# Performance work log

Hardware: AMD Instinct MI355X
Metric: run time of the kernel (lower is better)

## Reference

```python
import jax, jax.numpy as jnp
import numpy as np

N_NODES = 50000
N_EDGES = 800000
IN_DIM = 128
HID = 32
HEADS = 4


def _lin_init(key, fan_in, fan_out):
    k1, k2 = jax.random.split(key)
    s = 1.0 / np.sqrt(fan_in)
    W = jax.random.uniform(k1, (fan_in, fan_out), jnp.float32, -s, s)
    b = jax.random.uniform(k2, (fan_out,), jnp.float32, -s, s)
    return W, b


def setup_inputs() -> dict:
    key = jax.random.key(0)
    keys = jax.random.split(key, 12)
    x = jax.random.normal(keys[0], (N_NODES, IN_DIM), jnp.float32)
    edge_index = jax.random.randint(keys[1], (2, N_EDGES), 0, N_NODES, jnp.int64)

    # conv1: in_dim -> heads*hid (128 -> 4*32)
    Wq1, bq1 = _lin_init(keys[2], IN_DIM, HEADS * HID)
    Wk1, bk1 = _lin_init(keys[3], IN_DIM, HEADS * HID)
    Wv1, bv1 = _lin_init(keys[4], IN_DIM, HEADS * HID)
    Ws1, bs1 = _lin_init(keys[5], IN_DIM, HEADS * HID)
    # conv2: 128 -> 1*32
    Wq2, bq2 = _lin_init(keys[6], HEADS * HID, HID)
    Wk2, bk2 = _lin_init(keys[7], HEADS * HID, HID)
    Wv2, bv2 = _lin_init(keys[8], HEADS * HID, HID)
    Ws2, bs2 = _lin_init(keys[9], HEADS * HID, HID)
    # output linear: 32 -> 1
    Wo, bo = _lin_init(keys[10], HID, 1)

    return {
        "x": x, "edge_index": edge_index,
        "Wq1": Wq1, "bq1": bq1, "Wk1": Wk1, "bk1": bk1,
        "Wv1": Wv1, "bv1": bv1, "Ws1": Ws1, "bs1": bs1,
        "Wq2": Wq2, "bq2": bq2, "Wk2": Wk2, "bk2": bk2,
        "Wv2": Wv2, "bv2": bv2, "Ws2": Ws2, "bs2": bs2,
        "Wo": Wo, "bo": bo,
    }


def transformer_conv(x, edge_index, Wq, bq, Wk, bk, Wv, bv, Ws, bs, heads, d):
    # PyG TransformerConv (concat=True, root_weight=True, beta=False, no edge attr).
    n = x.shape[0]
    src, dst = edge_index[0], edge_index[1]  # message j(src) -> i(dst)
    q = (x @ Wq + bq).reshape(n, heads, d)
    k = (x @ Wk + bk).reshape(n, heads, d)
    v = (x @ Wv + bv).reshape(n, heads, d)
    # per-edge attention logits [E, heads]
    logits = (q[dst] * k[src]).sum(-1) / jnp.sqrt(jnp.float32(d))
    # segment softmax over incoming edges of each target node
    m = jax.ops.segment_max(logits, dst, num_segments=n)
    p = jnp.exp(logits - m[dst])
    denom = jax.ops.segment_sum(p, dst, num_segments=n)
    alpha = p / denom[dst]  # [E, heads]
    # weighted scatter-add of values
    msg = alpha[:, :, None] * v[src]  # [E, heads, d]
    aggr = jax.ops.segment_sum(msg, dst, num_segments=n).reshape(n, heads * d)
    return aggr + x @ Ws + bs  # root (skip) connection


def reference(x, edge_index,
              Wq1, bq1, Wk1, bk1, Wv1, bv1, Ws1, bs1,
              Wq2, bq2, Wk2, bk2, Wv2, bv2, Ws2, bs2,
              Wo, bo):
    h = transformer_conv(x, edge_index, Wq1, bq1, Wk1, bk1, Wv1, bv1, Ws1, bs1, HEADS, HID)
    h = jax.nn.relu(h)
    h = transformer_conv(h, edge_index, Wq2, bq2, Wk2, bk2, Wv2, bv2, Ws2, bs2, 1, HID)
    h = jax.nn.relu(h)
    g = h.mean(axis=0)  # [HID]
    return g @ Wo + bo  # [1]
```

## Files before the change

kernel.cpp:

```cpp
#include <hip/hip_runtime.h>
#include <math.h>

#define N_NODES 50000
#define N_EDGES 800000
#define NBK 196
#define BCAP 6144

typedef short short8 __attribute__((ext_vector_type(8)));
typedef float f32x4 __attribute__((ext_vector_type(4)));
typedef float f32x2 __attribute__((ext_vector_type(2)));

__device__ inline unsigned short f2bf(float v) {
  unsigned u = __float_as_uint(v);
  u += 0x7FFFu + ((u >> 16) & 1u);
  return (unsigned short)(u >> 16);
}
__device__ inline float bf2f(unsigned short b) {
  return __uint_as_float(((unsigned)b) << 16);
}
__device__ inline float bflo(unsigned u) { return __uint_as_float(u << 16); }
__device__ inline float bfhi(unsigned u) { return __uint_as_float(u & 0xFFFF0000u); }
__device__ inline unsigned char f2fp8(float v) {
  return (unsigned char)(__builtin_amdgcn_cvt_pk_fp8_f32(v, 0.f, 0, false) & 0xFF);
}
template <bool HI>
__device__ inline f32x2 fp8dec(unsigned u) {
  return __builtin_amdgcn_cvt_pk_f32_fp8(u, HI);
}

#define SCL 0.17677669529663687f

#define W1_B 256
#define W2_B 64
__global__ void prep_fused(const float* __restrict__ Wq1, const float* __restrict__ Wk1,
                           const float* __restrict__ Wv1, const float* __restrict__ Ws1,
                           const float* __restrict__ bq1, const float* __restrict__ bk1,
                           const float* __restrict__ bv1, const float* __restrict__ bs1,
                           const float* __restrict__ Wq2, const float* __restrict__ Wk2,
                           const float* __restrict__ Wv2, const float* __restrict__ Ws2,
                           const float* __restrict__ bq2, const float* __restrict__ bk2,
                           const float* __restrict__ bv2, const float* __restrict__ bs2,
                           unsigned short* __restrict__ Wt1, float* __restrict__ bcat1,
                           unsigned short* __restrict__ Wt2, float* __restrict__ bcat2,
                           const int* __restrict__ ei, int* __restrict__ bhist, int E) {
  const int b = blockIdx.x, tid = threadIdx.x;
  if (b < W1_B) {
    int i = b * 256 + tid;
    int c = i >> 7, k = i & 127;
    int mi = c >> 7, lc = c & 127;
    const float* W = (mi == 0) ? Wq1 : (mi == 1) ? Wk1 : (mi == 2) ? Wv1 : Ws1;
    float scl = (mi == 0) ? SCL : 1.f;
    Wt1[i] = f2bf(W[(size_t)k * 128 + lc] * scl);
    if (i < 512) {
      int bm = i >> 7, bl = i & 127;
      const float* bb = (bm == 0) ? bq1 : (bm == 1) ? bk1 : (bm == 2) ? bv1 : bs1;
      bcat1[i] = bb[bl] * ((bm == 0) ? SCL : 1.f);
    }
  } else if (b < W1_B + W2_B) {
    int i = (b - W1_B) * 256 + tid;
    int c = i >> 7, k = i & 127;
    int mi = c >> 5, lc = c & 31;
    const float* W = (mi == 0) ? Wq2 : (mi == 1) ? Wk2 : (mi == 2) ? Wv2 : Ws2;
    float scl = (mi == 0) ? SCL : 1.f;
    Wt2[i] = f2bf(W[(size_t)k * 32 + lc] * scl);
    if (i < 128) {
      int bm = i >> 5, bl = i & 31;
      const float* bb = (bm == 0) ? bq2 : (bm == 1) ? bk2 : (bm == 2) ? bv2 : bs2;
      bcat2[i] = bb[bl] * ((bm == 0) ? SCL : 1.f);
    }
  } else {
    __shared__ int h[NBK];
    for (int i = tid; i < NBK; i += 256) h[i] = 0;
    __syncthreads();
    int e = (b - W1_B - W2_B) * 4096 + tid;
#pragma unroll
    for (int p = 0; p < 16; ++p, e += 256)
      if (e < E) atomicAdd(&h[ei[E + e] >> 8], 1);
    __syncthreads();
    for (int i = tid; i < NBK; i += 256)
      if (h[i]) atomicAdd(&bhist[i], h[i]);
  }
}

__global__ void bucket_scan(const int* __restrict__ bhist, int* __restrict__ boff,
                            int* __restrict__ bcur) {
  __shared__ int s[256];
  int t = threadIdx.x;
  int v = (t < NBK) ? bhist[t] : 0;
  s[t] = v;
  __syncthreads();
#pragma unroll
  for (int off = 1; off < 256; off <<= 1) {
    int u = (t >= off) ? s[t - off] : 0;
    __syncthreads();
    s[t] += u;
    __syncthreads();
  }
  if (t < NBK) {
    int excl = s[t] - v;
    boff[t] = excl;
    bcur[t] = excl;
  }
  if (t == NBK - 1) boff[NBK] = s[t];
}

__global__ __launch_bounds__(256) void scatter_gemm1(
    const int* __restrict__ ei, int* __restrict__ bcur, int* __restrict__ ebuck, int E, int EB,
    const float* __restrict__ X, const unsigned short* __restrict__ Wt,
    const float* __restrict__ bcat, unsigned short* __restrict__ Q1b,
    unsigned short* __restrict__ SK1, unsigned char* __restrict__ KV8, int M) {
  __shared__ __align__(16) unsigned char L[3][64 * 272];
  const int tid = threadIdx.x;

  if ((int)blockIdx.x < EB) {
    int* lh = (int*)L[0];
    for (int i = tid; i < NBK; i += 256) lh[i] = 0;
    __syncthreads();
    const int e0 = blockIdx.x * 4096;
    int pks[16], bks[16];
#pragma unroll
    for (int p = 0; p < 16; ++p) {
      int e = e0 + p * 256 + tid;
      if (e < E) {
        int src = ei[e], dst = ei[E + e];
        pks[p] = (src << 8) | (dst & 255);
        bks[p] = dst >> 8;
        atomicAdd(&lh[bks[p]], 1);
      } else bks[p] = -1;
    }
    __syncthreads();
    for (int i = tid; i < NBK; i += 256)
      if (lh[i]) lh[i] = atomicAdd(&bcur[i], lh[i]);
    __syncthreads();
#pragma unroll
    for (int p = 0; p < 16; ++p) {
      if (bks[p] >= 0) {
        int slot = atomicAdd(&lh[bks[p]], 1);
        ebuck[slot] = pks[p];
      }
    }
    return;
  }

  unsigned short* As = (unsigned short*)L[0];
  const int bm = (blockIdx.x - EB) * 64;
  const int wave = tid >> 6, lane = tid & 63;
  const int lr = lane & 15, q = lane >> 4;

#pragma unroll
  for (int p = 0; p < 8; ++p) {
    int f = tid + p * 256;
    int row = f >> 5, c4 = f & 31;
    int gm = bm + row; if (gm >= M) gm = 0;
    float4 v = *(const float4*)(X + (size_t)gm * 128 + c4 * 4);
    ushort4 o;
    o.x = f2bf(v.x); o.y = f2bf(v.y); o.z = f2bf(v.z); o.w = f2bf(v.w);
    *(ushort4*)&As[row * 136 + c4 * 4] = o;
  }
  __syncthreads();

  const int colbase = wave * 128;
  f32x4 acc[4][8];
#pragma unroll
  for (int i = 0; i < 4; ++i)
#pragma unroll
    for (int j = 0; j < 8; ++j) acc[i][j] = (f32x4){0.f, 0.f, 0.f, 0.f};

#pragma unroll
  for (int ks = 0; ks < 4; ++ks) {
    short8 af[4];
#pragma unroll
    for (int i = 0; i < 4; ++i)
      af[i] = *(short8*)&As[(i * 16 + lr) * 136 + ks * 32 + q * 8];
#pragma unroll
    for (int j = 0; j < 8; ++j) {
      short8 bf = *(const short8*)(Wt + (size_t)(colbase + j * 16 + lr) * 128 + ks * 32 + q * 8);
#pragma unroll
      for (int i = 0; i < 4; ++i)
        acc[i][j] = __builtin_amdgcn_mfma_f32_16x16x32_bf16(af[i], bf, acc[i][j], 0, 0, 0);
    }
  }
  __syncthreads();

  float bj[8];
#pragma unroll
  for (int j = 0; j < 8; ++j) bj[j] = bcat[colbase + j * 16 + lr];

  if (wave == 0 || wave == 3) {
    unsigned short* Ls16 = (unsigned short*)((wave == 0) ? L[1] : L[0]);
#pragma unroll
    for (int i = 0; i < 4; ++i)
#pragma unroll
      for (int r = 0; r < 4; ++r) {
        int row = i * 16 + q * 4 + r;
#pragma unroll
        for (int j = 0; j < 8; ++j)
          Ls16[row * 136 + j * 16 + lr] = f2bf(acc[i][j][r] + bj[j]);
      }
  } else {
    unsigned char* KLs = L[2];
    const int voff = (wave == 2) ? 2 : 0;
#pragma unroll
    for (int i = 0; i < 4; ++i)
#pragma unroll
      for (int r = 0; r < 4; ++r) {
        int row = i * 16 + q * 4 + r;
#pragma unroll
        for (int j = 0; j < 8; ++j) {
          int d = j * 16 + lr;
          KLs[row * 272 + 4 * (d >> 1) + voff + (d & 1)] = f2fp8(acc[i][j][r] + bj[j]);
        }
      }
  }
  __syncthreads();

#pragma unroll
  for (int p = 0; p < 4; ++p) {
    int f = tid + p * 256;
    int row = f >> 4, u = f & 15;
    int gr = bm + row;
    if (gr < M) {
      *(uint4*)(Q1b + (size_t)gr * 128 + u * 8) = *(uint4*)&((unsigned short*)L[1])[row * 136 + u * 8];
      *(uint4*)(KV8 + (size_t)gr * 256 + u * 16) = *(uint4*)&L[2][row * 272 + u * 16];
      *(uint4*)(SK1 + (size_t)gr * 128 + u * 8) = *(uint4*)&((unsigned short*)L[0])[row * 136 + u * 8];
    }
  }
}

__global__ void bucket_csr(const int* __restrict__ ebuck, const int* __restrict__ boff,
                           int* __restrict__ rowptr, int* __restrict__ esrc, int N) {
  const int b = blockIdx.x;
  const int lo = boff[b], hi = boff[b + 1];
  const int cnt = hi - lo;
  __shared__ int hist[256];
  __shared__ int cur[256];
  __shared__ int sorted[BCAP];
  const int t = threadIdx.x;
  hist[t] = 0;
  __syncthreads();
  for (int i = t; i < cnt; i += 256) atomicAdd(&hist[ebuck[lo + i] & 255], 1);
  __syncthreads();
  int v = hist[t];
  sorted[t] = v;
  __syncthreads();
#pragma unroll
  for (int off = 1; off < 256; off <<= 1) {
    int u = (t >= off) ? sorted[t - off] : 0;
    __syncthreads();
    sorted[t] += u;
    __syncthreads();
  }
  int excl = sorted[t] - v;
  cur[t] = excl;
  int node = b * 256 + t;
  if (node <= N) rowptr[node] = lo + excl;
  __syncthreads();
  for (int i = t; i < cnt; i += 256) {
    int pk = ebuck[lo + i];
    int slot = atomicAdd(&cur[pk & 255], 1);
    if (slot < BCAP) sorted[slot] = pk;
    else esrc[lo + slot] = pk & 0xFFFFFF00;
  }
  __syncthreads();
  int lim = cnt < BCAP ? cnt : BCAP;
  for (int i = t; i < lim; i += 256) esrc[lo + i] = sorted[i] & 0xFFFFFF00;
}

__global__ __launch_bounds__(256) void gemm2(
    const unsigned short* __restrict__ Ab, const unsigned short* __restrict__ Wt,
    const float* __restrict__ bcat, unsigned char* __restrict__ C2b, int M) {
  __shared__ __align__(16) unsigned short As[64 * 136];
  __shared__ __align__(16) unsigned char Lsb[64 * 272];
  const int bm = blockIdx.x * 64;
  const int tid = threadIdx.x, wave = tid >> 6, lane = tid & 63;
  const int lr = lane & 15, q = lane >> 4;

#pragma unroll
  for (int p = 0; p < 4; ++p) {
    int f = tid + p * 256;
    int row = f >> 4, chunk = f & 15;
    int gm = bm + row; if (gm >= M) gm = 0;
    uint4 v = *(const uint4*)(Ab + (size_t)gm * 128 + chunk * 8);
    *(uint4*)&As[row * 136 + chunk * 8] = v;
  }
  __syncthreads();

  f32x4 acc[4][2];
#pragma unroll
  for (int i = 0; i < 4; ++i)
#pragma unroll
    for (int j = 0; j < 2; ++j) acc[i][j] = (f32x4){0.f, 0.f, 0.f, 0.f};

#pragma unroll
  for (int ks = 0; ks < 4; ++ks) {
    short8 af[4];
#pragma unroll
    for (int i = 0; i < 4; ++i)
      af[i] = *(short8*)&As[(i * 16 + lr) * 136 + ks * 32 + q * 8];
#pragma unroll
    for (int j = 0; j < 2; ++j) {
      short8 bf = *(const short8*)(Wt + (size_t)(wave * 32 + j * 16 + lr) * 128 + ks * 32 + q * 8);
#pragma unroll
      for (int i = 0; i < 4; ++i)
        acc[i][j] = __builtin_amdgcn_mfma_f32_16x16x32_bf16(af[i], bf, acc[i][j], 0, 0, 0);
    }
  }

  float bj[2];
#pragma unroll
  for (int j = 0; j < 2; ++j) bj[j] = bcat[wave * 32 + j * 16 + lr];
#pragma unroll
  for (int i = 0; i < 4; ++i)
#pragma unroll
    for (int r = 0; r < 4; ++r) {
      int row = i * 16 + q * 4 + r;
#pragma unroll
      for (int j = 0; j < 2; ++j) {
        int c = wave * 32 + j * 16 + lr;
        float val = acc[i][j][r] + bj[j];
        if (c < 32) {
          *(unsigned short*)&Lsb[row * 272 + 2 * c] = f2bf(val);
        } else if (c < 64) {
          int d = c - 32;
          Lsb[row * 272 + 64 + 4 * (d >> 1) + (d & 1)] = f2fp8(val);
        } else if (c < 96) {
          int d = c - 64;
          Lsb[row * 272 + 64 + 4 * (d >> 1) + 2 + (d & 1)] = f2fp8(val);
        } else {
          *(unsigned short*)&Lsb[row * 272 + 192 + 2 * (c - 96)] = f2bf(val);
        }
      }
    }
  __syncthreads();
#pragma unroll
  for (int p = 0; p < 16; ++p) {
    int idx = tid + p * 256;
    int row = idx >> 6, u = idx & 63;
    int gr = bm + row;
    if (gr < M) *(unsigned*)(C2b + (size_t)gr * 256 + u * 4) = *(const unsigned*)&Lsb[row * 272 + u * 4];
  }
}

__global__ void node_attn1(const int* __restrict__ rowptr, const int* __restrict__ esrc,
                           const unsigned short* __restrict__ Qb,
                           const unsigned char* __restrict__ KV8,
                           const unsigned short* __restrict__ SK, unsigned short* __restrict__ Hb,
                           int n) {
  int node = (blockIdx.x * blockDim.x + threadIdx.x) >> 6;
  int lane = threadIdx.x & 63;
  if (node >= n) return;
  const int half = lane >> 5, ll = lane & 31;
  const int r0 = rowptr[node], r1 = rowptr[node + 1];
  uint2 qq = *(const uint2*)(Qb + (size_t)node * 128 + ll * 4);
  const float q0 = bflo(qq.x), q1 = bfhi(qq.x), q2 = bflo(qq.y), q3 = bfhi(qq.y);
  float l = 0.f, a0 = 0.f, a1 = 0.f, a2 = 0.f, a3 = 0.f;
  const unsigned char* kvb = KV8 + ll * 8;
  int j = r0;
  for (; j + 8 <= r1; j += 8) {
    int e = j + half * 4;
    int s0 = esrc[e], s1 = esrc[e + 1], s2 = esrc[e + 2], s3 = esrc[e + 3];
    uint2 u0 = *(const uint2*)(kvb + s0);
    uint2 u1 = *(const uint2*)(kvb + s1);
    uint2 u2 = *(const uint2*)(kvb + s2);
    uint2 u3 = *(const uint2*)(kvb + s3);
    f32x2 k0a = fp8dec<false>(u0.x), k0b = fp8dec<false>(u0.y);
    f32x2 k1a = fp8dec<false>(u1.x), k1b = fp8dec<false>(u1.y);
    f32x2 k2a = fp8dec<false>(u2.x), k2b = fp8dec<false>(u2.y);
    f32x2 k3a = fp8dec<false>(u3.x), k3b = fp8dec<false>(u3.y);
    float d0 = q0 * k0a.x + q1 * k0a.y + q2 * k0b.x + q3 * k0b.y;
    float d1 = q0 * k1a.x + q1 * k1a.y + q2 * k1b.x + q3 * k1b.y;
    float d2 = q0 * k2a.x + q1 * k2a.y + q2 * k2b.x + q3 * k2b.y;
    float d3 = q0 * k3a.x + q1 * k3a.y + q2 * k3b.x + q3 * k3b.y;
#pragma unroll
    for (int msk = 1; msk <= 4; msk <<= 1) {
      d0 += __shfl_xor(d0, msk);
      d1 += __shfl_xor(d1, msk);
      d2 += __shfl_xor(d2, msk);
      d3 += __shfl_xor(d3, msk);
    }
    float p0 = __expf(d0), p1 = __expf(d1), p2 = __expf(d2), p3 = __expf(d3);
    l += (p0 + p1) + (p2 + p3);
    f32x2 v0a = fp8dec<true>(u0.x), v0b = fp8dec<true>(u0.y);
    f32x2 v1a = fp8dec<true>(u1.x), v1b = fp8dec<true>(u1.y);
    f32x2 v2a = fp8dec<true>(u2.x), v2b = fp8dec<true>(u2.y);
    f32x2 v3a = fp8dec<true>(u3.x), v3b = fp8dec<true>(u3.y);
    a0 += p0 * v0a.x + p1 * v1a.x + p2 * v2a.x + p3 * v3a.x;
    a1 += p0 * v0a.y + p1 * v1a.y + p2 * v2a.y + p3 * v3a.y;
    a2 += p0 * v0b.x + p1 * v1b.x + p2 * v2b.x + p3 * v3b.x;
    a3 += p0 * v0b.y + p1 * v1b.y + p2 * v2b.y + p3 * v3b.y;
  }
  for (; j < r1; j += 4) {
    int eA = j + half * 2, eB = eA + 1;
    bool vA = eA < r1, vB = eB < r1;
    int sA = esrc[vA ? eA : r0];
    int sB = esrc[vB ? eB : r0];
    uint2 ua = *(const uint2*)(kvb + sA);
    uint2 ub = *(const uint2*)(kvb + sB);
    f32x2 ka1 = fp8dec<false>(ua.x), ka2 = fp8dec<false>(ua.y);
    f32x2 kb1 = fp8dec<false>(ub.x), kb2 = fp8dec<false>(ub.y);
    float dA = q0 * ka1.x + q1 * ka1.y + q2 * ka2.x + q3 * ka2.y;
    float dB = q0 * kb1.x + q1 * kb1.y + q2 * kb2.x + q3 * kb2.y;
#pragma unroll
    for (int msk = 1; msk <= 4; msk <<= 1) {
      dA += __shfl_xor(dA, msk);
      dB += __shfl_xor(dB, msk);
    }
    float pA = vA ? __expf(dA) : 0.f;
    float pB = vB ? __expf(dB) : 0.f;
    l += pA + pB;
    f32x2 va1 = fp8dec<true>(ua.x), va2 = fp8dec<true>(ua.y);
    f32x2 vb1 = fp8dec<true>(ub.x), vb2 = fp8dec<true>(ub.y);
    a0 += pA * va1.x + pB * vb1.x;
    a1 += pA * va1.y + pB * vb1.y;
    a2 += pA * va2.x + pB * vb2.x;
    a3 += pA * va2.y + pB * vb2.y;
  }
  l  += __shfl_xor(l, 32);
  a0 += __shfl_xor(a0, 32);
  a1 += __shfl_xor(a1, 32);
  a2 += __shfl_xor(a2, 32);
  a3 += __shfl_xor(a3, 32);
  float inv = (l > 0.f) ? 1.f / l : 0.f;
  if (half == 0) {
    uint2 sk = *(const uint2*)(SK + (size_t)node * 128 + ll * 4);
    float o0 = fmaxf(bflo(sk.x) + a0 * inv, 0.f);
    float o1 = fmaxf(bfhi(sk.x) + a1 * inv, 0.f);
    float o2 = fmaxf(bflo(sk.y) + a2 * inv, 0.f);
    float o3 = fmaxf(bfhi(sk.y) + a3 * inv, 0.f);
    uint2 hb;
    hb.x = ((unsigned)f2bf(o1) << 16) | (unsigned)f2bf(o0);
    hb.y = ((unsigned)f2bf(o3) << 16) | (unsigned)f2bf(o2);
    *(uint2*)(Hb + (size_t)node * 128 + ll * 4) = hb;
  }
}

__global__ void node_attn2(const int* __restrict__ rowptr, const int* __restrict__ esrc,
                           const unsigned char* __restrict__ C2b, const float* __restrict__ Wo,
                           float* __restrict__ pblock, int n) {
  __shared__ float ps[4];
  int node = (blockIdx.x * blockDim.x + threadIdx.x) >> 6;
  int lane = threadIdx.x & 63;
  int wave = threadIdx.x >> 6;
  const int g = lane >> 4, gl = lane & 15;
  float t = 0.f;
  if (node < n) {
    const int r0 = rowptr[node], r1 = rowptr[node + 1];
    unsigned qu = *(const unsigned*)(C2b + (size_t)node * 256 + gl * 4);
    const float q0 = bflo(qu), q1 = bfhi(qu);
    float l = 0.f, a0 = 0.f, a1 = 0.f;
    const unsigned char* kvb = C2b + 64 + gl * 4;
    int j = r0;
    for (; j + 8 <= r1; j += 8) {
      int e = j + g * 2;
      int s0 = esrc[e], s1 = esrc[e + 1];
      unsigned u0 = *(const unsigned*)(kvb + s0);
      unsigned u1 = *(const unsigned*)(kvb + s1);
      f32x2 k0 = fp8dec<false>(u0), k1 = fp8dec<false>(u1);
      float d0 = q0 * k0.x + q1 * k0.y;
      float d1 = q0 * k1.x + q1 * k1.y;
#pragma unroll
      for (int msk = 1; msk <= 8; msk <<= 1) {
        d0 += __shfl_xor(d0, msk);
        d1 += __shfl_xor(d1, msk);
      }
      float p0 = __expf(d0), p1 = __expf(d1);
      l += p0 + p1;
      f32x2 v0 = fp8dec<true>(u0), v1 = fp8dec<true>(u1);
      a0 += p0 * v0.x + p1 * v1.x;
      a1 += p0 * v0.y + p1 * v1.y;
    }
    for (; j < r1; j += 4) {
      bool v = (j + g) < r1;
      int s = esrc[v ? j + g : r0];
      unsigned u = *(const unsigned*)(kvb + s);
      f32x2 kd = fp8dec<false>(u);
      float d = q0 * kd.x + q1 * kd.y;
#pragma unroll
      for (int msk = 1; msk <= 8; msk <<= 1) d += __shfl_xor(d, msk);
      float p = v ? __expf(d) : 0.f;
      l += p;
      f32x2 vd = fp8dec<true>(u);
      a0 += p * vd.x;
      a1 += p * vd.y;
    }
#pragma unroll
    for (int msk = 16; msk <= 32; msk <<= 1) {
      l  += __shfl_xor(l, msk);
      a0 += __shfl_xor(a0, msk);
      a1 += __shfl_xor(a1, msk);
    }
    float inv = (l > 0.f) ? 1.f / l : 0.f;
    unsigned hu = *(const unsigned*)(C2b + (size_t)node * 256 + 192 + gl * 4);
    float o0 = fmaxf(bflo(hu) + a0 * inv, 0.f);
    float o1 = fmaxf(bfhi(hu) + a1 * inv, 0.f);
    t = o0 * Wo[2 * gl] + o1 * Wo[2 * gl + 1];
#pragma unroll
    for (int msk = 1; msk <= 8; msk <<= 1) t += __shfl_xor(t, msk);
  }
  if (lane == 0) ps[wave] = t;
  __syncthreads();
  if (threadIdx.x == 0) pblock[blockIdx.x] = ps[0] + ps[1] + ps[2] + ps[3];
}

__global__ void final_out(const float* __restrict__ pblock, const float* __restrict__ bo,
                          float* __restrict__ out, int nb, float invN) {
  __shared__ float s[256];
  float acc = 0.f;
  for (int i = threadIdx.x; i < nb; i += 256) acc += pblock[i];
  s[threadIdx.x] = acc;
  __syncthreads();
  for (int off = 128; off >= 1; off >>= 1) {
    if (threadIdx.x < off) s[threadIdx.x] += s[threadIdx.x + off];
    __syncthreads();
  }
  if (threadIdx.x == 0) out[0] = s[0] * invN + bo[0];
}

extern "C" void kernel_launch(void* const* d_in, const int* in_sizes, int n_in,
                              void* d_out, int out_size, void* d_ws, size_t ws_size,
                              hipStream_t stream) {
  const float* x   = (const float*)d_in[0];
  const int*   ei  = (const int*)d_in[1];
  const float* Wq1 = (const float*)d_in[2];  const float* bq1 = (const float*)d_in[3];
  const float* Wk1 = (const float*)d_in[4];  const float* bk1 = (const float*)d_in[5];
  const float* Wv1 = (const float*)d_in[6];  const float* bv1 = (const float*)d_in[7];
  const float* Ws1 = (const float*)d_in[8];  const float* bs1 = (const float*)d_in[9];
  const float* Wq2 = (const float*)d_in[10]; const float* bq2 = (const float*)d_in[11];
  const float* Wk2 = (const float*)d_in[12]; const float* bk2 = (const float*)d_in[13];
  const float* Wv2 = (const float*)d_in[14]; const float* bv2 = (const float*)d_in[15];
  const float* Ws2 = (const float*)d_in[16]; const float* bs2 = (const float*)d_in[17];
  const float* Wo  = (const float*)d_in[18]; const float* bo  = (const float*)d_in[19];

  char* ws = (char*)d_ws;
  const int N = N_NODES, E = N_EDGES;
  const int GB = (N + 63) / 64;
  const int EB = (E + 4095) / 4096;
  const int AB = (N * 64) / 256;

  unsigned short* Q1b = (unsigned short*)(ws + 0);
  unsigned short* SK1 = (unsigned short*)(ws + 12800000);
  unsigned char*  KV1 = (unsigned char*)(ws + 25600000);
  unsigned short* H1b = (unsigned short*)(ws + 51200000);
  unsigned char*  C2  = (unsigned char*)(ws + 64000000);
  int* rowptr = (int*)(ws + 89600000);
  int* esrc   = (int*)(ws + 89900032);
  int* bhist  = (int*)(ws + 93100032);
  int* boff   = (int*)(ws + 93101056);
  int* bcur   = (int*)(ws + 93102080);
  unsigned short* Wt1   = (unsigned short*)(ws + 93103104);
  unsigned short* Wt2   = (unsigned short*)(ws + 93234176);
  float*          bcat1 = (float*)(ws + 93266944);
  float*          bcat2 = (float*)(ws + 93268992);
  float*          pblock = (float*)(ws + 93269504);
  int*            ebuck = (int*)(ws + 93319552);

  float* out = (float*)d_out;

  dim3 blk(256);

  hipMemsetAsync(bhist, 0, NBK * sizeof(int), stream);

  prep_fused<<<dim3(W1_B + W2_B + EB), blk, 0, stream>>>(
      Wq1, Wk1, Wv1, Ws1, bq1, bk1, bv1, bs1,
      Wq2, Wk2, Wv2, Ws2, bq2, bk2, bv2, bs2,
      Wt1, bcat1, Wt2, bcat2, ei, bhist, E);

  bucket_scan<<<dim3(1), blk, 0, stream>>>(bhist, boff, bcur);

  scatter_gemm1<<<dim3(EB + GB), blk, 0, stream>>>(
      ei, bcur, ebuck, E, EB, x, Wt1, bcat1, Q1b, SK1, KV1, N);

  bucket_csr<<<dim3(NBK), blk, 0, stream>>>(ebuck, boff, rowptr, esrc, N);

  node_attn1<<<dim3(AB), blk, 0, stream>>>(rowptr, esrc, Q1b, KV1, SK1, H1b, N);

  gemm2<<<dim3(GB), blk, 0, stream>>>(H1b, Wt2, bcat2, C2, N);

  node_attn2<<<dim3(AB), blk, 0, stream>>>(rowptr, esrc, C2, Wo, pblock, N);

  final_out<<<dim3(1), blk, 0, stream>>>(pblock, bo, out, AB, 1.0f / (float)N);
}
```

Before: 249.9 us.

## Split GEMM1 columns across two blocks and store K and V as separate planes

The first-layer projection GEMM now launches two blocks per 64-row tile, each computing half of the 512 output columns. This halves the per-wave accumulator array and shrinks the LDS footprint, aiming for higher occupancy and more parallelism in the fused scatter/GEMM kernel. The cost is that each row tile of X is loaded and converted to bf16 twice. The fp8 K/V buffer changes from interleaved per-lane pairs to a K plane and a V plane within each 256-byte row, so node_attn1 now issues two 4-byte gathers per edge instead of one 8-byte gather.

```diff
diff --git a/kernel.cpp b/kernel.cpp
--- a/kernel.cpp
+++ b/kernel.cpp
@@ -109,11 +109,12 @@
     const float* __restrict__ X, const unsigned short* __restrict__ Wt,
     const float* __restrict__ bcat, unsigned short* __restrict__ Q1b,
     unsigned short* __restrict__ SK1, unsigned char* __restrict__ KV8, int M) {
-  __shared__ __align__(16) unsigned char L[3][64 * 272];
+  __shared__ __align__(16) unsigned short As[64 * 136];
+  __shared__ __align__(16) unsigned char Bs[64 * 144];
   const int tid = threadIdx.x;
 
   if ((int)blockIdx.x < EB) {
-    int* lh = (int*)L[0];
+    int* lh = (int*)As;
     for (int i = tid; i < NBK; i += 256) lh[i] = 0;
     __syncthreads();
     const int e0 = blockIdx.x * 4096;
@@ -142,8 +143,9 @@
     return;
   }
 
-  unsigned short* As = (unsigned short*)L[0];
-  const int bm = (blockIdx.x - EB) * 64;
+  const int idx = blockIdx.x - EB;
+  const int gb = idx >> 1, half = idx & 1;
+  const int bm = gb * 64;
   const int wave = tid >> 6, lane = tid & 63;
   const int lr = lane & 15, q = lane >> 4;
 
@@ -159,12 +161,14 @@
   }
   __syncthreads();
 
-  const int colbase = wave * 128;
-  f32x4 acc[4][8];
+  const int colbase = half * 256 + ((wave >= 2) ? 128 : 0) + (wave & 1) * 64;
+  const bool tobytes = (half == 0) ? (wave >= 2) : (wave < 2);
+
+  f32x4 acc[4][4];
 #pragma unroll
   for (int i = 0; i < 4; ++i)
 #pragma unroll
-    for (int j = 0; j < 8; ++j) acc[i][j] = (f32x4){0.f, 0.f, 0.f, 0.f};
+    for (int j = 0; j < 4; ++j) acc[i][j] = (f32x4){0.f, 0.f, 0.f, 0.f};
 
 #pragma unroll
   for (int ks = 0; ks < 4; ++ks) {
@@ -173,7 +177,7 @@
     for (int i = 0; i < 4; ++i)
       af[i] = *(short8*)&As[(i * 16 + lr) * 136 + ks * 32 + q * 8];
 #pragma unroll
-    for (int j = 0; j < 8; ++j) {
+    for (int j = 0; j < 4; ++j) {
       short8 bf = *(const short8*)(Wt + (size_t)(colbase + j * 16 + lr) * 128 + ks * 32 + q * 8);
 #pragma unroll
       for (int i = 0; i < 4; ++i)
@@ -182,48 +186,42 @@
   }
   __syncthreads();
 
-  float bj[8];
-#pragma unroll
-  for (int j = 0; j < 8; ++j) bj[j] = bcat[colbase + j * 16 + lr];
-
-  if (wave == 0 || wave == 3) {
-    unsigned short* Ls16 = (unsigned short*)((wave == 0) ? L[1] : L[0]);
-#pragma unroll
-    for (int i = 0; i < 4; ++i)
-#pragma unroll
-      for (int r = 0; r < 4; ++r) {
-        int row = i * 16 + q * 4 + r;
-#pragma unroll
-        for (int j = 0; j < 8; ++j)
-          Ls16[row * 136 + j * 16 + lr] = f2bf(acc[i][j][r] + bj[j]);
+  float bj[4];
+#pragma unroll
+  for (int j = 0; j < 4; ++j) bj[j] = bcat[colbase + j * 16 + lr];
+
+#pragma unroll
+  for (int i = 0; i < 4; ++i)
+#pragma unroll
+    for (int r = 0; r < 4; ++r) {
+      int row = i * 16 + q * 4 + r;
+#pragma unroll
+      for (int j = 0; j < 4; ++j) {
+        int lc = (wave & 1) * 64 + j * 16 + lr;
+        float val = acc[i][j][r] + bj[j];
+        if (tobytes) Bs[row * 144 + lc] = f2fp8(val);
+        else         As[row * 136 + lc] = f2bf(val);
       }
-  } else {
-    unsigned char* KLs = L[2];
-    const int voff = (wave == 2) ? 2 : 0;
-#pragma unroll
-    for (int i = 0; i < 4; ++i)
-#pragma unroll
-      for (int r = 0; r < 4; ++r) {
-        int row = i * 16 + q * 4 + r;
-#pragma unroll
-        for (int j = 0; j < 8; ++j) {
-          int d = j * 16 + lr;
-          KLs[row * 272 + 4 * (d >> 1) + voff + (d & 1)] = f2fp8(acc[i][j][r] + bj[j]);
-        }
-      }
-  }
-  __syncthreads();
-
+    }
+  __syncthreads();
+
+  unsigned short* out16 = half ? SK1 : Q1b;
+  const int plane = half ? 128 : 0;
 #pragma unroll
   for (int p = 0; p < 4; ++p) {
     int f = tid + p * 256;
     int row = f >> 4, u = f & 15;
     int gr = bm + row;
-    if (gr < M) {
-      *(uint4*)(Q1b + (size_t)gr * 128 + u * 8) = *(uint4*)&((unsigned short*)L[1])[row * 136 + u * 8];
-      *(uint4*)(KV8 + (size_t)gr * 256 + u * 16) = *(uint4*)&L[2][row * 272 + u * 16];
-      *(uint4*)(SK1 + (size_t)gr * 128 + u * 8) = *(uint4*)&((unsigned short*)L[0])[row * 136 + u * 8];
-    }
+    if (gr < M)
+      *(uint4*)(out16 + (size_t)gr * 128 + u * 8) = *(uint4*)&As[row * 136 + u * 8];
+  }
+#pragma unroll
+  for (int p = 0; p < 2; ++p) {
+    int f = tid + p * 256;
+    int row = f >> 3, u = f & 7;
+    int gr = bm + row;
+    if (gr < M)
+      *(uint4*)(KV8 + (size_t)gr * 256 + plane + u * 16) = *(uint4*)&Bs[row * 144 + u * 16];
   }
 }
 
@@ -354,19 +352,24 @@
   uint2 qq = *(const uint2*)(Qb + (size_t)node * 128 + ll * 4);
   const float q0 = bflo(qq.x), q1 = bfhi(qq.x), q2 = bflo(qq.y), q3 = bfhi(qq.y);
   float l = 0.f, a0 = 0.f, a1 = 0.f, a2 = 0.f, a3 = 0.f;
-  const unsigned char* kvb = KV8 + ll * 8;
+  const unsigned char* kb = KV8 + ll * 4;
+  const unsigned char* vb = KV8 + 128 + ll * 4;
   int j = r0;
   for (; j + 8 <= r1; j += 8) {
     int e = j + half * 4;
     int s0 = esrc[e], s1 = esrc[e + 1], s2 = esrc[e + 2], s3 = esrc[e + 3];
-    uint2 u0 = *(const uint2*)(kvb + s0);
-    uint2 u1 = *(const uint2*)(kvb + s1);
-    uint2 u2 = *(const uint2*)(kvb + s2);
-    uint2 u3 = *(const uint2*)(kvb + s3);
-    f32x2 k0a = fp8dec<false>(u0.x), k0b = fp8dec<false>(u0.y);
-    f32x2 k1a = fp8dec<false>(u1.x), k1b = fp8dec<false>(u1.y);
-    f32x2 k2a = fp8dec<false>(u2.x), k2b = fp8dec<false>(u2.y);
-    f32x2 k3a = fp8dec<false>(u3.x), k3b = fp8dec<false>(u3.y);
+    unsigned kk0 = *(const unsigned*)(kb + s0);
+    unsigned kk1 = *(const unsigned*)(kb + s1);
+    unsigned kk2 = *(const unsigned*)(kb + s2);
+    unsigned kk3 = *(const unsigned*)(kb + s3);
+    unsigned vv0 = *(const unsigned*)(vb + s0);
+    unsigned vv1 = *(const unsigned*)(vb + s1);
+    unsigned vv2 = *(const unsigned*)(vb + s2);
+    unsigned vv3 = *(const unsigned*)(vb + s3);
+    f32x2 k0a = fp8dec<false>(kk0), k0b = fp8dec<true>(kk0);
+    f32x2 k1a = fp8dec<false>(kk1), k1b = fp8dec<true>(kk1);
+    f32x2 k2a = fp8dec<false>(kk2), k2b = fp8dec<true>(kk2);
+    f32x2 k3a = fp8dec<false>(kk3), k3b = fp8dec<true>(kk3);
     float d0 = q0 * k0a.x + q1 * k0a.y + q2 * k0b.x + q3 * k0b.y;
     float d1 = q0 * k1a.x + q1 * k1a.y + q2 * k1b.x + q3 * k1b.y;
     float d2 = q0 * k2a.x + q1 * k2a.y + q2 * k2b.x + q3 * k2b.y;
@@ -380,10 +383,10 @@
     }
     float p0 = __expf(d0), p1 = __expf(d1), p2 = __expf(d2), p3 = __expf(d3);
     l += (p0 + p1) + (p2 + p3);
-    f32x2 v0a = fp8dec<true>(u0.x), v0b = fp8dec<true>(u0.y);
-    f32x2 v1a = fp8dec<true>(u1.x), v1b = fp8dec<true>(u1.y);
-    f32x2 v2a = fp8dec<true>(u2.x), v2b = fp8dec<true>(u2.y);
-    f32x2 v3a = fp8dec<true>(u3.x), v3b = fp8dec<true>(u3.y);
+    f32x2 v0a = fp8dec<false>(vv0), v0b = fp8dec<true>(vv0);
+    f32x2 v1a = fp8dec<false>(vv1), v1b = fp8dec<true>(vv1);
+    f32x2 v2a = fp8dec<false>(vv2), v2b = fp8dec<true>(vv2);
+    f32x2 v3a = fp8dec<false>(vv3), v3b = fp8dec<true>(vv3);
     a0 += p0 * v0a.x + p1 * v1a.x + p2 * v2a.x + p3 * v3a.x;
     a1 += p0 * v0a.y + p1 * v1a.y + p2 * v2a.y + p3 * v3a.y;
     a2 += p0 * v0b.x + p1 * v1b.x + p2 * v2b.x + p3 * v3b.x;
@@ -394,10 +397,12 @@
     bool vA = eA < r1, vB = eB < r1;
     int sA = esrc[vA ? eA : r0];
     int sB = esrc[vB ? eB : r0];
-    uint2 ua = *(const uint2*)(kvb + sA);
-    uint2 ub = *(const uint2*)(kvb + sB);
-    f32x2 ka1 = fp8dec<false>(ua.x), ka2 = fp8dec<false>(ua.y);
-    f32x2 kb1 = fp8dec<false>(ub.x), kb2 = fp8dec<false>(ub.y);
+    unsigned kkA = *(const unsigned*)(kb + sA);
+    unsigned kkB = *(const unsigned*)(kb + sB);
+    unsigned vvA = *(const unsigned*)(vb + sA);
+    unsigned vvB = *(const unsigned*)(vb + sB);
+    f32x2 ka1 = fp8dec<false>(kkA), ka2 = fp8dec<true>(kkA);
+    f32x2 kb1 = fp8dec<false>(kkB), kb2 = fp8dec<true>(kkB);
     float dA = q0 * ka1.x + q1 * ka1.y + q2 * ka2.x + q3 * ka2.y;
     float dB = q0 * kb1.x + q1 * kb1.y + q2 * kb2.x + q3 * kb2.y;
 #pragma unroll
@@ -408,8 +413,8 @@
     float pA = vA ? __expf(dA) : 0.f;
     float pB = vB ? __expf(dB) : 0.f;
     l += pA + pB;
-    f32x2 va1 = fp8dec<true>(ua.x), va2 = fp8dec<true>(ua.y);
-    f32x2 vb1 = fp8dec<true>(ub.x), vb2 = fp8dec<true>(ub.y);
+    f32x2 va1 = fp8dec<false>(vvA), va2 = fp8dec<true>(vvA);
+    f32x2 vb1 = fp8dec<false>(vvB), vb2 = fp8dec<true>(vvB);
     a0 += pA * va1.x + pB * vb1.x;
     a1 += pA * va1.y + pB * vb1.y;
     a2 += pA * va2.x + pB * vb2.x;
@@ -567,7 +572,7 @@
 
   bucket_scan<<<dim3(1), blk, 0, stream>>>(bhist, boff, bcur);
 
-  scatter_gemm1<<<dim3(EB + GB), blk, 0, stream>>>(
+  scatter_gemm1<<<dim3(EB + 2 * GB), blk, 0, stream>>>(
       ei, bcur, ebuck, E, EB, x, Wt1, bcat1, Q1b, SK1, KV1, N);
 
   bucket_csr<<<dim3(NBK), blk, 0, stream>>>(ebuck, boff, rowptr, esrc, N);
```

New measurement: 254.2 us. About the same (+1.7%).
